# Performance work log

Hardware: AMD Instinct MI355X
Metric: run time of the kernel (lower is better)

The kernel has to match this reference:

```python
import jax, jax.numpy as jnp
import numpy as np

B, C, H, W = 4, 256, 64, 64
C8 = C // 8


def setup_inputs() -> dict:
    key = jax.random.key(0)
    ks = jax.random.split(key, 7)
    return {
        "x": jax.random.normal(ks[0], (B, C, H, W), dtype=jnp.float32),
        "Wq": jax.random.normal(ks[1], (C8, C), dtype=jnp.float32) * 0.05,
        "bq": jax.random.normal(ks[2], (C8,), dtype=jnp.float32) * 0.05,
        "Wk": jax.random.normal(ks[3], (C8, C), dtype=jnp.float32) * 0.05,
        "bk": jax.random.normal(ks[4], (C8,), dtype=jnp.float32) * 0.05,
        "Wv": jax.random.normal(ks[5], (C, C), dtype=jnp.float32) * 0.05,
        "bv": jax.random.normal(ks[6], (C,), dtype=jnp.float32) * 0.05,
        "gamma": jnp.zeros((1,), dtype=jnp.float32),
    }


def reference(x, Wq, bq, Wk, bk, Wv, bv, gamma):
    b, c, h, w = x.shape
    n = h * w
    xf = x.reshape(b, c, n)  # [B, C, N]
    # 1x1 convs == per-pixel linear maps over channels
    q = jnp.einsum('oc,bcn->bon', Wq, xf) + bq[None, :, None]  # [B, C/8, N]
    k = jnp.einsum('oc,bcn->bon', Wk, xf) + bk[None, :, None]  # [B, C/8, N]
    v = jnp.einsum('oc,bcn->bon', Wv, xf) + bv[None, :, None]  # [B, C, N]
    # s[b,i,j] = q_i . k_j ; torch softmax over dim=-2 (the i axis)
    s = jnp.einsum('bci,bcj->bij', q, k)  # [B, N, N]
    attn_T = jax.nn.softmax(s, axis=-2)
    # o[b,c,j] = sum_i v[b,c,i] * attn_T[b,i,j]
    o = jnp.einsum('bci,bij->bcj', v, attn_T)  # [B, C, N]
    return x + gamma[0] * o.reshape(b, c, h, w)
```

## Files before the change

### kernel.cpp

```cpp
#include <hip/hip_runtime.h>
#include <hip/hip_bf16.h>


typedef float  f32x16 __attribute__((ext_vector_type(16)));
typedef float  f32x4  __attribute__((ext_vector_type(4)));
typedef short  s16x8  __attribute__((ext_vector_type(8)));
typedef unsigned int u32;
typedef unsigned int u32x4 __attribute__((ext_vector_type(4)));

__device__ __forceinline__ s16x8 ld16(const ushort* p) {
  return *reinterpret_cast<const s16x8*>(p);
}
__device__ __forceinline__ ushort f2bf(float f) {
  return (ushort)((__float_as_uint(f) + 0x8000u) >> 16);
}
__device__ __forceinline__ u32 cvt_pk_bf16(float lo, float hi) {
  u32 r;
  asm("v_cvt_pk_bf16_f32 %0, %1, %2" : "=v"(r) : "v"(lo), "v"(hi));
  return r;
}

__global__ void wf_kernel(const float* __restrict__ Wq, const float* __restrict__ Wk,
                          const float* __restrict__ Wv,
                          const float* __restrict__ bq, const float* __restrict__ bk,
                          const float* __restrict__ bv, ushort* __restrict__ WF) {
  const int blk = blockIdx.x;
  const int ob = blk / 17, kb = blk % 17;
  const int t = threadIdx.x;
  const int l = t >> 3, e = t & 7;
  const int l31 = l & 31, g = l >> 5;
  const int o = ob * 32 + l31;
  float val;
  if (kb == 16) {
    float bias = (ob == 0) ? bq[l31] : (ob == 1) ? bk[l31] : bv[o - 64];
    val = (g == 0 && e == 0) ? bias : 0.f;
  } else {
    const int c = kb * 16 + (e & 3) + ((e >> 2) << 3) + (g << 2);
    val = (ob == 0) ? Wq[l31 * 256 + c]
        : (ob == 1) ? Wk[l31 * 256 + c]
                    : Wv[(o - 64) * 256 + c];
  }
  WF[((size_t)blk * 64 + l) * 8 + e] = f2bf(val);
}

__global__ __launch_bounds__(640) void proj_kernel(
    const float* __restrict__ x, const ushort* __restrict__ WF,
    ushort* __restrict__ qA, ushort* __restrict__ kB, ushort* __restrict__ vA) {
  __shared__ ushort xbf[17 * 1024];
  __shared__ ushort obuf[20480];
  const int bid = blockIdx.x;
  const int b = bid >> 6, w = bid & 63;
  const int n0 = w << 6;
  const int t = threadIdx.x;

  const float* xb = x + (size_t)(b * 256) * 4096 + n0;
  #pragma unroll
  for (int kk = 0; kk < 7; ++kk) {
    int idx = t + kk * 640;
    if (idx < 4096) {
      int c = idx >> 4, nq = idx & 15;
      f32x4 xv = *reinterpret_cast<const f32x4*>(xb + (size_t)c * 4096 + nq * 4);
      int kb = c >> 4, r = c & 15;
      int gg = (r >> 2) & 1, ee = (r & 3) + ((r >> 3) << 2);
      #pragma unroll
      for (int u = 0; u < 4; ++u) {
        int n = nq * 4 + u;
        xbf[kb * 1024 + ((n >> 5) * 2 + gg) * 256 + (n & 31) * 8 + ee] = f2bf(xv[u]);
      }
    }
  }
  for (int u = t; u < 1024; u += 640) {
    int gg = (u >> 8) & 1, ee = u & 7;
    xbf[16 * 1024 + u] = (gg == 0 && ee == 0) ? (ushort)0x3F80 : (ushort)0;
  }
  __syncthreads();

  const int l = t & 63;
  const int wv = __builtin_amdgcn_readfirstlane(t >> 6);
  const int l31 = l & 31, g = l >> 5;

  s16x8 wf[17];
  #pragma unroll
  for (int kb = 0; kb < 17; ++kb)
    wf[kb] = ld16(WF + ((size_t)(wv * 17 + kb) * 64 + l) * 8);

  f32x16 acc[2];
  #pragma unroll
  for (int nb = 0; nb < 2; ++nb)
    #pragma unroll
    for (int r = 0; r < 16; ++r) acc[nb][r] = 0.f;

  #pragma unroll
  for (int nb = 0; nb < 2; ++nb)
    #pragma unroll
    for (int kb = 0; kb < 17; ++kb)
      acc[nb] = __builtin_amdgcn_mfma_f32_32x32x16_bf16(
          wf[kb], ld16(xbf + kb * 1024 + (nb * 2 + g) * 256 + l31 * 8), acc[nb], 0, 0, 0);

  if (wv < 2) {
    const int obase = wv * 2048;
    #pragma unroll
    for (int nb = 0; nb < 2; ++nb)
      #pragma unroll
      for (int r = 0; r < 16; ++r)
        obuf[obase + (nb * 4 + (r >> 3) * 2 + g) * 256 + l31 * 8 + (r & 3) + (((r >> 2) & 1) << 2)]
            = f2bf(acc[nb][r]);
  } else {
    const int gv = (l31 >> 2) & 1;
    const int ev = (l31 & 3) + (((l31 >> 3) & 1) << 2);
    #pragma unroll
    for (int nb = 0; nb < 2; ++nb) {
      const int fi = (nb * 2 + (l31 >> 4)) * 2 + gv;
      #pragma unroll
      for (int r = 0; r < 16; ++r) {
        const int c = (wv - 2) * 32 + (r & 3) + ((r >> 2) << 3) + (g << 2);
        obuf[4096 + (fi * 256 + c) * 8 + ev] = f2bf(acc[nb][r]);
      }
    }
  }
  __syncthreads();

  const size_t qbase = (size_t)(b * 64 + w) * 2048;
  const size_t vbase = ((size_t)b * 512 + w * 8) * 2048;
  #pragma unroll
  for (int kk = 0; kk < 4; ++kk) {
    int ci = t + kk * 640;
    int off = ci * 8;
    s16x8 val = ld16(obuf + off);
    ushort* dst = (off < 2048) ? (qA + qbase + off)
                : (off < 4096) ? (kB + qbase + off - 2048)
                               : (vA + vbase + off - 4096);
    *reinterpret_cast<s16x8*>(dst) = val;
  }
}

__global__ __launch_bounds__(512, 2) void attn_kernel(
    const ushort* __restrict__ qA, const ushort* __restrict__ kB, const ushort* __restrict__ vA,
    const float* __restrict__ x, const float* __restrict__ gamma, float* __restrict__ out) {
  __shared__ ushort pls[2 * 8 * 2 * 512];
  __shared__ float lsr[4][2][64];
  const int bid = blockIdx.x;
  const int b = bid & 3;
  const int jt = bid >> 2;
  const int j0 = jt << 6;
  const int t = threadIdx.x;
  const int l = t & 63;
  const int wv = __builtin_amdgcn_readfirstlane(t >> 6);
  const int l31 = l & 31, g = l >> 5;
  const float gm = gamma[0];

  if (wv >= 4) {
    const int sw = wv - 4;
    s16x8 kf00, kf01, kf10, kf11;
    {
      const size_t kb0 = (size_t)((b * 64 + jt) * 8 + g) * 256 + l31 * 8;
      kf00 = ld16(kB + kb0);
      kf01 = ld16(kB + kb0 + 512);
      kf10 = ld16(kB + kb0 + 1024);
      kf11 = ld16(kB + kb0 + 1536);
    }
    float lsum0 = 1e-30f, lsum1 = 1e-30f;
    s16x8 qf0, qf1;
    {
      const size_t qb = (size_t)((b * 64 + (sw >> 1)) * 8 + (sw & 1) * 4 + g) * 256 + l31 * 8;
      qf0 = ld16(qA + qb);
      qf1 = ld16(qA + qb + 512);
    }
    for (int reg = 0; reg <= 32; ++reg) {
      if (reg < 32) {
        const int wi = reg, buf = wi & 1;
        f32x16 s0, s1;
        #pragma unroll
        for (int r = 0; r < 16; ++r) { s0[r] = 0.f; s1[r] = 0.f; }
        __builtin_amdgcn_s_setprio(1);
        s0 = __builtin_amdgcn_mfma_f32_32x32x16_bf16(qf0, kf00, s0, 0, 0, 0);
        s0 = __builtin_amdgcn_mfma_f32_32x32x16_bf16(qf1, kf01, s0, 0, 0, 0);
        s1 = __builtin_amdgcn_mfma_f32_32x32x16_bf16(qf0, kf10, s1, 0, 0, 0);
        s1 = __builtin_amdgcn_mfma_f32_32x32x16_bf16(qf1, kf11, s1, 0, 0, 0);
        __builtin_amdgcn_s_setprio(0);
        if (wi < 31) {
          const size_t qb = (size_t)((b * 64 + (wi + 1) * 2 + (sw >> 1)) * 8 + (sw & 1) * 4 + g) * 256 + l31 * 8;
          qf0 = ld16(qA + qb);
          qf1 = ld16(qA + qb + 512);
        }
        float p0[16], p1[16], ls0 = 0.f, ls1 = 0.f;
        #pragma unroll
        for (int r = 0; r < 16; ++r) {
          p0[r] = __builtin_amdgcn_exp2f(__builtin_fmaf(s0[r], 1.4426950408889634f, -24.0f));
          p1[r] = __builtin_amdgcn_exp2f(__builtin_fmaf(s1[r], 1.4426950408889634f, -24.0f));
          ls0 += p0[r];
          ls1 += p1[r];
        }
        lsum0 += ls0;
        lsum1 += ls1;
        u32x4 w00, w01, w10, w11;
        #pragma unroll
        for (int q = 0; q < 4; ++q) {
          w00[q] = cvt_pk_bf16(p0[2 * q],     p0[2 * q + 1]);
          w01[q] = cvt_pk_bf16(p0[8 + 2 * q], p0[8 + 2 * q + 1]);
          w10[q] = cvt_pk_bf16(p1[2 * q],     p1[2 * q + 1]);
          w11[q] = cvt_pk_bf16(p1[8 + 2 * q], p1[8 + 2 * q + 1]);
        }
        ushort* p00 = pls + ((buf * 16 + (2 * sw + 0) * 2 + 0) * 512) + l * 8;
        ushort* p01 = pls + ((buf * 16 + (2 * sw + 1) * 2 + 0) * 512) + l * 8;
        ushort* p10 = pls + ((buf * 16 + (2 * sw + 0) * 2 + 1) * 512) + l * 8;
        ushort* p11 = pls + ((buf * 16 + (2 * sw + 1) * 2 + 1) * 512) + l * 8;
        *reinterpret_cast<s16x8*>(p00) = __builtin_bit_cast(s16x8, w00);
        *reinterpret_cast<s16x8*>(p01) = __builtin_bit_cast(s16x8, w01);
        *reinterpret_cast<s16x8*>(p10) = __builtin_bit_cast(s16x8, w10);
        *reinterpret_cast<s16x8*>(p11) = __builtin_bit_cast(s16x8, w11);
      } else {
        lsr[sw][0][l] = lsum0;
        lsr[sw][1][l] = lsum1;
      }
      asm volatile("s_waitcnt lgkmcnt(0)" ::: "memory");
      __builtin_amdgcn_s_barrier();
      __builtin_amdgcn_sched_barrier(0);
    }
  } else {
    const int pv = wv;
    const ushort* vbase = vA + ((size_t)(b * 512 + g) * 256 + pv * 64 + l31) * 8;
    f32x16 acc[2][2];
    #pragma unroll
    for (int cg = 0; cg < 2; ++cg)
      #pragma unroll
      for (int jb = 0; jb < 2; ++jb)
        #pragma unroll
        for (int r = 0; r < 16; ++r) acc[cg][jb][r] = 0.f;
    s16x8 vf[8][2];
    for (int reg = 0; reg <= 32; ++reg) {
      if (reg == 0) {
        #pragma unroll
        for (int m = 0; m < 8; ++m) {
          vf[m][0] = ld16(vbase + (size_t)m * 4096);
          vf[m][1] = ld16(vbase + (size_t)m * 4096 + 256);
        }
      } else {
        const int wi = reg - 1, buf = wi & 1;
        #pragma unroll
        for (int m = 0; m < 8; ++m) {
          s16x8 pf0 = ld16(pls + ((buf * 16 + m * 2 + 0) * 512) + l * 8);
          s16x8 pf1 = ld16(pls + ((buf * 16 + m * 2 + 1) * 512) + l * 8);
          acc[0][0] = __builtin_amdgcn_mfma_f32_32x32x16_bf16(vf[m][0], pf0, acc[0][0], 0, 0, 0);
          acc[1][0] = __builtin_amdgcn_mfma_f32_32x32x16_bf16(vf[m][1], pf0, acc[1][0], 0, 0, 0);
          acc[0][1] = __builtin_amdgcn_mfma_f32_32x32x16_bf16(vf[m][0], pf1, acc[0][1], 0, 0, 0);
          acc[1][1] = __builtin_amdgcn_mfma_f32_32x32x16_bf16(vf[m][1], pf1, acc[1][1], 0, 0, 0);
          if (reg < 32) {
            vf[m][0] = ld16(vbase + (size_t)(reg * 8 + m) * 4096);
            vf[m][1] = ld16(vbase + (size_t)(reg * 8 + m) * 4096 + 256);
          }
        }
      }
      __builtin_amdgcn_s_barrier();
      __builtin_amdgcn_sched_barrier(0);
    }
    #pragma unroll
    for (int jb = 0; jb < 2; ++jb) {
      float tot = 0.f;
      #pragma unroll
      for (int sw2 = 0; sw2 < 4; ++sw2)
        tot += lsr[sw2][jb][l31] + lsr[sw2][jb][l31 + 32];
      const float sc = gm / tot;
      #pragma unroll
      for (int cg = 0; cg < 2; ++cg) {
        #pragma unroll
        for (int r = 0; r < 16; ++r) {
          const int c = pv * 64 + cg * 32 + (r & 3) + ((r >> 2) << 3) + (g << 2);
          const size_t idx = (size_t)(b * 256 + c) * 4096 + j0 + jb * 32 + l31;
          out[idx] = __builtin_fmaf(sc, acc[cg][jb][r], x[idx]);
        }
      }
    }
  }
}

extern "C" void kernel_launch(void* const* d_in, const int* in_sizes, int n_in,
                              void* d_out, int out_size, void* d_ws, size_t ws_size,
                              hipStream_t stream) {
  const float* x     = (const float*)d_in[0];
  const float* Wq    = (const float*)d_in[1];
  const float* bq    = (const float*)d_in[2];
  const float* Wk    = (const float*)d_in[3];
  const float* bk    = (const float*)d_in[4];
  const float* Wv    = (const float*)d_in[5];
  const float* bv    = (const float*)d_in[6];
  const float* gamma = (const float*)d_in[7];
  float* out = (float*)d_out;

  char* ws = (char*)d_ws;
  ushort* WF = (ushort*)(ws);
  ushort* qA = (ushort*)(ws + 262144);
  ushort* kB = (ushort*)(ws + 262144 + 1048576);
  ushort* vA = (ushort*)(ws + 262144 + 2097152);

  wf_kernel  <<<170, 512, 0, stream>>>(Wq, Wk, Wv, bq, bk, bv, WF);
  proj_kernel<<<256, 640, 0, stream>>>(x, WF, qA, kB, vA);
  attn_kernel<<<256, 512, 0, stream>>>(qA, kB, vA, x, gamma, out);
}
```

Before: 62.80 us.

## Halve per-block tile width to double grid size for proj and attn kernels

Both the projection and attention kernels now process 32 columns per block instead of 64, doubling the launch grid to 512 blocks so all CUs get work. LDS buffers and accumulators shrink accordingly, and attn_kernel's launch bounds rise to allow four blocks per CU. The PV loop also prefetches the next P fragment from LDS before issuing MFMAs. In exchange, each K/Q and V tile is reloaded by twice as many blocks, and each block does less MFMA work per barrier, so synchronization overhead per FLOP rises.

```diff
diff --git a/kernel.cpp b/kernel.cpp
--- a/kernel.cpp
+++ b/kernel.cpp
@@ -46,32 +46,31 @@
 __global__ __launch_bounds__(640) void proj_kernel(
     const float* __restrict__ x, const ushort* __restrict__ WF,
     ushort* __restrict__ qA, ushort* __restrict__ kB, ushort* __restrict__ vA) {
-  __shared__ ushort xbf[17 * 1024];
-  __shared__ ushort obuf[20480];
+  __shared__ ushort xbf[17 * 512];
+  __shared__ ushort obuf[10240];
   const int bid = blockIdx.x;
-  const int b = bid >> 6, w = bid & 63;
-  const int n0 = w << 6;
+  const int b = bid >> 7, w = bid & 127;
+  const int n0 = w << 5;
   const int t = threadIdx.x;
 
   const float* xb = x + (size_t)(b * 256) * 4096 + n0;
   #pragma unroll
-  for (int kk = 0; kk < 7; ++kk) {
+  for (int kk = 0; kk < 4; ++kk) {
     int idx = t + kk * 640;
-    if (idx < 4096) {
-      int c = idx >> 4, nq = idx & 15;
+    if (idx < 2048) {
+      int c = idx >> 3, nq = idx & 7;
       f32x4 xv = *reinterpret_cast<const f32x4*>(xb + (size_t)c * 4096 + nq * 4);
       int kb = c >> 4, r = c & 15;
       int gg = (r >> 2) & 1, ee = (r & 3) + ((r >> 3) << 2);
       #pragma unroll
       for (int u = 0; u < 4; ++u) {
         int n = nq * 4 + u;
-        xbf[kb * 1024 + ((n >> 5) * 2 + gg) * 256 + (n & 31) * 8 + ee] = f2bf(xv[u]);
-      }
-    }
-  }
-  for (int u = t; u < 1024; u += 640) {
-    int gg = (u >> 8) & 1, ee = u & 7;
-    xbf[16 * 1024 + u] = (gg == 0 && ee == 0) ? (ushort)0x3F80 : (ushort)0;
+        xbf[kb * 512 + gg * 256 + n * 8 + ee] = f2bf(xv[u]);
+      }
+    }
+  }
+  if (t < 512) {
+    xbf[16 * 512 + t] = (((t >> 8) == 0) && ((t & 7) == 0)) ? (ushort)0x3F80 : (ushort)0;
   }
   __syncthreads();
 
@@ -84,65 +83,57 @@
   for (int kb = 0; kb < 17; ++kb)
     wf[kb] = ld16(WF + ((size_t)(wv * 17 + kb) * 64 + l) * 8);
 
-  f32x16 acc[2];
-  #pragma unroll
-  for (int nb = 0; nb < 2; ++nb)
-    #pragma unroll
-    for (int r = 0; r < 16; ++r) acc[nb][r] = 0.f;
-
-  #pragma unroll
-  for (int nb = 0; nb < 2; ++nb)
-    #pragma unroll
-    for (int kb = 0; kb < 17; ++kb)
-      acc[nb] = __builtin_amdgcn_mfma_f32_32x32x16_bf16(
-          wf[kb], ld16(xbf + kb * 1024 + (nb * 2 + g) * 256 + l31 * 8), acc[nb], 0, 0, 0);
+  f32x16 acc;
+  #pragma unroll
+  for (int r = 0; r < 16; ++r) acc[r] = 0.f;
+  #pragma unroll
+  for (int kb = 0; kb < 17; ++kb)
+    acc = __builtin_amdgcn_mfma_f32_32x32x16_bf16(
+        wf[kb], ld16(xbf + kb * 512 + g * 256 + l31 * 8), acc, 0, 0, 0);
 
   if (wv < 2) {
-    const int obase = wv * 2048;
-    #pragma unroll
-    for (int nb = 0; nb < 2; ++nb)
-      #pragma unroll
-      for (int r = 0; r < 16; ++r)
-        obuf[obase + (nb * 4 + (r >> 3) * 2 + g) * 256 + l31 * 8 + (r & 3) + (((r >> 2) & 1) << 2)]
-            = f2bf(acc[nb][r]);
+    const int obase = wv * 1024;
+    #pragma unroll
+    for (int r = 0; r < 16; ++r)
+      obuf[obase + ((r >> 3) * 2 + g) * 256 + l31 * 8 + (r & 3) + (((r >> 2) & 1) << 2)]
+          = f2bf(acc[r]);
   } else {
     const int gv = (l31 >> 2) & 1;
     const int ev = (l31 & 3) + (((l31 >> 3) & 1) << 2);
-    #pragma unroll
-    for (int nb = 0; nb < 2; ++nb) {
-      const int fi = (nb * 2 + (l31 >> 4)) * 2 + gv;
-      #pragma unroll
-      for (int r = 0; r < 16; ++r) {
-        const int c = (wv - 2) * 32 + (r & 3) + ((r >> 2) << 3) + (g << 2);
-        obuf[4096 + (fi * 256 + c) * 8 + ev] = f2bf(acc[nb][r]);
-      }
+    const int fi = (l31 >> 4) * 2 + gv;
+    #pragma unroll
+    for (int r = 0; r < 16; ++r) {
+      const int c = (wv - 2) * 32 + (r & 3) + ((r >> 2) << 3) + (g << 2);
+      obuf[2048 + (fi * 256 + c) * 8 + ev] = f2bf(acc[r]);
     }
   }
   __syncthreads();
 
-  const size_t qbase = (size_t)(b * 64 + w) * 2048;
-  const size_t vbase = ((size_t)b * 512 + w * 8) * 2048;
-  #pragma unroll
-  for (int kk = 0; kk < 4; ++kk) {
+  const size_t qbase = ((size_t)(b * 64 + (w >> 1)) * 8 + (w & 1) * 4) * 256;
+  const size_t vbase = ((size_t)b * 512 + w * 4) * 2048;
+  #pragma unroll
+  for (int kk = 0; kk < 2; ++kk) {
     int ci = t + kk * 640;
-    int off = ci * 8;
-    s16x8 val = ld16(obuf + off);
-    ushort* dst = (off < 2048) ? (qA + qbase + off)
-                : (off < 4096) ? (kB + qbase + off - 2048)
-                               : (vA + vbase + off - 4096);
-    *reinterpret_cast<s16x8*>(dst) = val;
-  }
-}
-
-__global__ __launch_bounds__(512, 2) void attn_kernel(
+    if (ci < 1280) {
+      int off = ci * 8;
+      s16x8 val = ld16(obuf + off);
+      ushort* dst = (off < 1024) ? (qA + qbase + off)
+                  : (off < 2048) ? (kB + qbase + off - 1024)
+                                 : (vA + vbase + off - 2048);
+      *reinterpret_cast<s16x8*>(dst) = val;
+    }
+  }
+}
+
+__global__ __launch_bounds__(512, 4) void attn_kernel(
     const ushort* __restrict__ qA, const ushort* __restrict__ kB, const ushort* __restrict__ vA,
     const float* __restrict__ x, const float* __restrict__ gamma, float* __restrict__ out) {
-  __shared__ ushort pls[2 * 8 * 2 * 512];
-  __shared__ float lsr[4][2][64];
+  __shared__ ushort pls[2 * 8 * 512];
+  __shared__ float lsr[4][64];
   const int bid = blockIdx.x;
   const int b = bid & 3;
   const int jt = bid >> 2;
-  const int j0 = jt << 6;
+  const int j0 = jt << 5;
   const int t = threadIdx.x;
   const int l = t & 63;
   const int wv = __builtin_amdgcn_readfirstlane(t >> 6);
@@ -151,15 +142,13 @@
 
   if (wv >= 4) {
     const int sw = wv - 4;
-    s16x8 kf00, kf01, kf10, kf11;
+    s16x8 kf0, kf1;
     {
-      const size_t kb0 = (size_t)((b * 64 + jt) * 8 + g) * 256 + l31 * 8;
-      kf00 = ld16(kB + kb0);
-      kf01 = ld16(kB + kb0 + 512);
-      kf10 = ld16(kB + kb0 + 1024);
-      kf11 = ld16(kB + kb0 + 1536);
-    }
-    float lsum0 = 1e-30f, lsum1 = 1e-30f;
+      const size_t kb0 = (size_t)((b * 64 + (jt >> 1)) * 8 + (jt & 1) * 4 + g) * 256 + l31 * 8;
+      kf0 = ld16(kB + kb0);
+      kf1 = ld16(kB + kb0 + 512);
+    }
+    float lsum = 1e-30f;
     s16x8 qf0, qf1;
     {
       const size_t qb = (size_t)((b * 64 + (sw >> 1)) * 8 + (sw & 1) * 4 + g) * 256 + l31 * 8;
@@ -169,49 +158,37 @@
     for (int reg = 0; reg <= 32; ++reg) {
       if (reg < 32) {
         const int wi = reg, buf = wi & 1;
-        f32x16 s0, s1;
-        #pragma unroll
-        for (int r = 0; r < 16; ++r) { s0[r] = 0.f; s1[r] = 0.f; }
+        f32x16 s0;
+        #pragma unroll
+        for (int r = 0; r < 16; ++r) s0[r] = 0.f;
         __builtin_amdgcn_s_setprio(1);
-        s0 = __builtin_amdgcn_mfma_f32_32x32x16_bf16(qf0, kf00, s0, 0, 0, 0);
-        s0 = __builtin_amdgcn_mfma_f32_32x32x16_bf16(qf1, kf01, s0, 0, 0, 0);
-        s1 = __builtin_amdgcn_mfma_f32_32x32x16_bf16(qf0, kf10, s1, 0, 0, 0);
-        s1 = __builtin_amdgcn_mfma_f32_32x32x16_bf16(qf1, kf11, s1, 0, 0, 0);
+        s0 = __builtin_amdgcn_mfma_f32_32x32x16_bf16(qf0, kf0, s0, 0, 0, 0);
+        s0 = __builtin_amdgcn_mfma_f32_32x32x16_bf16(qf1, kf1, s0, 0, 0, 0);
         __builtin_amdgcn_s_setprio(0);
         if (wi < 31) {
           const size_t qb = (size_t)((b * 64 + (wi + 1) * 2 + (sw >> 1)) * 8 + (sw & 1) * 4 + g) * 256 + l31 * 8;
           qf0 = ld16(qA + qb);
           qf1 = ld16(qA + qb + 512);
         }
-        float p0[16], p1[16], ls0 = 0.f, ls1 = 0.f;
+        float p0[16], ls = 0.f;
         #pragma unroll
         for (int r = 0; r < 16; ++r) {
           p0[r] = __builtin_amdgcn_exp2f(__builtin_fmaf(s0[r], 1.4426950408889634f, -24.0f));
-          p1[r] = __builtin_amdgcn_exp2f(__builtin_fmaf(s1[r], 1.4426950408889634f, -24.0f));
-          ls0 += p0[r];
-          ls1 += p1[r];
-        }
-        lsum0 += ls0;
-        lsum1 += ls1;
-        u32x4 w00, w01, w10, w11;
+          ls += p0[r];
+        }
+        lsum += ls;
+        u32x4 wlo, whi;
         #pragma unroll
         for (int q = 0; q < 4; ++q) {
-          w00[q] = cvt_pk_bf16(p0[2 * q],     p0[2 * q + 1]);
-          w01[q] = cvt_pk_bf16(p0[8 + 2 * q], p0[8 + 2 * q + 1]);
-          w10[q] = cvt_pk_bf16(p1[2 * q],     p1[2 * q + 1]);
-          w11[q] = cvt_pk_bf16(p1[8 + 2 * q], p1[8 + 2 * q + 1]);
-        }
-        ushort* p00 = pls + ((buf * 16 + (2 * sw + 0) * 2 + 0) * 512) + l * 8;
-        ushort* p01 = pls + ((buf * 16 + (2 * sw + 1) * 2 + 0) * 512) + l * 8;
-        ushort* p10 = pls + ((buf * 16 + (2 * sw + 0) * 2 + 1) * 512) + l * 8;
-        ushort* p11 = pls + ((buf * 16 + (2 * sw + 1) * 2 + 1) * 512) + l * 8;
-        *reinterpret_cast<s16x8*>(p00) = __builtin_bit_cast(s16x8, w00);
-        *reinterpret_cast<s16x8*>(p01) = __builtin_bit_cast(s16x8, w01);
-        *reinterpret_cast<s16x8*>(p10) = __builtin_bit_cast(s16x8, w10);
-        *reinterpret_cast<s16x8*>(p11) = __builtin_bit_cast(s16x8, w11);
+          wlo[q] = cvt_pk_bf16(p0[2 * q],     p0[2 * q + 1]);
+          whi[q] = cvt_pk_bf16(p0[8 + 2 * q], p0[8 + 2 * q + 1]);
+        }
+        ushort* plo = pls + ((buf * 8 + 2 * sw + 0) * 512) + l * 8;
+        ushort* phi = pls + ((buf * 8 + 2 * sw + 1) * 512) + l * 8;
+        *reinterpret_cast<s16x8*>(plo) = __builtin_bit_cast(s16x8, wlo);
+        *reinterpret_cast<s16x8*>(phi) = __builtin_bit_cast(s16x8, whi);
       } else {
-        lsr[sw][0][l] = lsum0;
-        lsr[sw][1][l] = lsum1;
+        lsr[sw][l] = lsum;
       }
       asm volatile("s_waitcnt lgkmcnt(0)" ::: "memory");
       __builtin_amdgcn_s_barrier();
@@ -220,13 +197,11 @@
   } else {
     const int pv = wv;
     const ushort* vbase = vA + ((size_t)(b * 512 + g) * 256 + pv * 64 + l31) * 8;
-    f32x16 acc[2][2];
+    f32x16 acc[2];
     #pragma unroll
     for (int cg = 0; cg < 2; ++cg)
       #pragma unroll
-      for (int jb = 0; jb < 2; ++jb)
-        #pragma unroll
-        for (int r = 0; r < 16; ++r) acc[cg][jb][r] = 0.f;
+      for (int r = 0; r < 16; ++r) acc[cg][r] = 0.f;
     s16x8 vf[8][2];
     for (int reg = 0; reg <= 32; ++reg) {
       if (reg == 0) {
@@ -237,14 +212,15 @@
         }
       } else {
         const int wi = reg - 1, buf = wi & 1;
+        const ushort* pb = pls + (size_t)buf * 8 * 512 + l * 8;
+        s16x8 nf = ld16(pb);
         #pragma unroll
         for (int m = 0; m < 8; ++m) {
-          s16x8 pf0 = ld16(pls + ((buf * 16 + m * 2 + 0) * 512) + l * 8);
-          s16x8 pf1 = ld16(pls + ((buf * 16 + m * 2 + 1) * 512) + l * 8);
-          acc[0][0] = __builtin_amdgcn_mfma_f32_32x32x16_bf16(vf[m][0], pf0, acc[0][0], 0, 0, 0);
-          acc[1][0] = __builtin_amdgcn_mfma_f32_32x32x16_bf16(vf[m][1], pf0, acc[1][0], 0, 0, 0);
-          acc[0][1] = __builtin_amdgcn_mfma_f32_32x32x16_bf16(vf[m][0], pf1, acc[0][1], 0, 0, 0);
-          acc[1][1] = __builtin_amdgcn_mfma_f32_32x32x16_bf16(vf[m][1], pf1, acc[1][1], 0, 0, 0);
+          s16x8 cf = nf;
+          if (m < 7) nf = ld16(pb + (m + 1) * 512);
+          __builtin_amdgcn_sched_barrier(0);
+          acc[0] = __builtin_amdgcn_mfma_f32_32x32x16_bf16(vf[m][0], cf, acc[0], 0, 0, 0);
+          acc[1] = __builtin_amdgcn_mfma_f32_32x32x16_bf16(vf[m][1], cf, acc[1], 0, 0, 0);
           if (reg < 32) {
             vf[m][0] = ld16(vbase + (size_t)(reg * 8 + m) * 4096);
             vf[m][1] = ld16(vbase + (size_t)(reg * 8 + m) * 4096 + 256);
@@ -254,21 +230,18 @@
       __builtin_amdgcn_s_barrier();
       __builtin_amdgcn_sched_barrier(0);
     }
-    #pragma unroll
-    for (int jb = 0; jb < 2; ++jb) {
-      float tot = 0.f;
+    float tot = 0.f;
+    #pragma unroll
+    for (int sw2 = 0; sw2 < 4; ++sw2)
+      tot += lsr[sw2][l31] + lsr[sw2][l31 + 32];
+    const float sc = gm / tot;
+    #pragma unroll
+    for (int cg = 0; cg < 2; ++cg) {
       #pragma unroll
-      for (int sw2 = 0; sw2 < 4; ++sw2)
-        tot += lsr[sw2][jb][l31] + lsr[sw2][jb][l31 + 32];
-      const float sc = gm / tot;
-      #pragma unroll
-      for (int cg = 0; cg < 2; ++cg) {
-        #pragma unroll
-        for (int r = 0; r < 16; ++r) {
-          const int c = pv * 64 + cg * 32 + (r & 3) + ((r >> 2) << 3) + (g << 2);
-          const size_t idx = (size_t)(b * 256 + c) * 4096 + j0 + jb * 32 + l31;
-          out[idx] = __builtin_fmaf(sc, acc[cg][jb][r], x[idx]);
-        }
+      for (int r = 0; r < 16; ++r) {
+        const int c = pv * 64 + cg * 32 + (r & 3) + ((r >> 2) << 3) + (g << 2);
+        const size_t idx = (size_t)(b * 256 + c) * 4096 + j0 + l31;
+        out[idx] = __builtin_fmaf(sc, acc[cg][r], x[idx]);
       }
     }
   }
@@ -294,6 +267,6 @@
   ushort* vA = (ushort*)(ws + 262144 + 2097152);
 
   wf_kernel  <<<170, 512, 0, stream>>>(Wq, Wk, Wv, bq, bk, bv, WF);
-  proj_kernel<<<256, 640, 0, stream>>>(x, WF, qA, kB, vA);
-  attn_kernel<<<256, 512, 0, stream>>>(qA, kB, vA, x, gamma, out);
-}
+  proj_kernel<<<512, 640, 0, stream>>>(x, WF, qA, kB, vA);
+  attn_kernel<<<512, 512, 0, stream>>>(qA, kB, vA, x, gamma, out);
+}
```

Result: slower. 74.19 us (+18.1%).
